# Performance work log

Measured on AMD Instinct MI355X. Metric: run time of the kernel, lower is better.

Reference implementation:

```python
import jax, jax.numpy as jnp
import numpy as np

VEC_DIM = 32
RANK = 2
D = H = W = 40


def setup_inputs() -> dict:
    key = jax.random.key(0)
    k1, k2, k3 = jax.random.split(key, 3)
    volume = jax.random.normal(k1, (D, H, W, VEC_DIM), dtype=jnp.float32)
    # M is nn.Linear(m, m, bias=False) init uniform(-0.5, 0.5)
    M_weight = jax.random.uniform(k2, (VEC_DIM, VEC_DIM), jnp.float32, -0.5, 0.5)
    # P init uniform(-0.1, 0.1)
    P = jax.random.uniform(k3, (VEC_DIM, VEC_DIM), jnp.float32, -0.1, 0.1)
    return {"volume": volume, "M_weight": M_weight, "P": P}


def reference(volume, M_weight, P):
    m = volume.shape[-1]
    r = RANK
    # --- extract_windows: linear mode (step=1), rank_mode='drop', rank_op='avg' ---
    # mean over each r x r x r cubic window == sum-pool / r^3 (VALID padding = drop)
    pooled = jax.lax.reduce_window(
        volume, 0.0, jax.lax.add,
        window_dimensions=(r, r, r, 1),
        window_strides=(1, 1, 1, 1),
        padding="VALID",
    ) / float(r ** 3)  # [Dp, Hp, Wp, m]
    Dp, Hp, Wp = pooled.shape[:3]
    vecs = pooled.reshape(-1, m)  # [B, m], B = Dp*Hp*Wp (window order: k1 outer, k3 inner)
    k1 = jnp.arange(Dp, dtype=jnp.float32)
    k2 = jnp.arange(Hp, dtype=jnp.float32)
    k3 = jnp.arange(Wp, dtype=jnp.float32)
    k1g, k2g, k3g = jnp.meshgrid(k1, k2, k3, indexing="ij")
    k1f, k2f, k3f = k1g.ravel(), k2g.ravel(), k3g.ravel()  # [B]
    # --- batch_compute_Nk ---
    # periods[i, j] = i*m + j + 2
    periods = (jnp.arange(m, dtype=jnp.float32)[:, None] * m
               + jnp.arange(m, dtype=jnp.float32)[None, :] + 2.0)  # [m, m]
    two_pi = 2.0 * jnp.pi
    inv_p = two_pi / periods  # [m, m]
    # phi[b, i, j] = cos(2pi*k1/p) * cos(2pi*k2/p) * cos(2pi*k3/p)
    phi = (jnp.cos(k1f[:, None, None] * inv_p)
           * jnp.cos(k2f[:, None, None] * inv_p)
           * jnp.cos(k3f[:, None, None] * inv_p))  # [B, m, m]
    x = vecs @ M_weight.T  # nn.Linear: x = v W^T, [B, m]
    Nk = jnp.einsum("bj,ij,bij->bi", x, P, phi)  # [B, m]
    return Nk
```

## Files before the change

### kernel.cpp

```cpp
#include <hip/hip_runtime.h>
#include <math.h>

constexpr int DV = 40;
constexpr int NP = 39;
constexpr int VD = 32;
constexpr float TWO_PI = 6.28318530717958647692f;

__global__ __launch_bounds__(256) void ndk_kernel(
    const float* __restrict__ vol,
    const float* __restrict__ Mw,
    const float* __restrict__ P,
    float* __restrict__ out)
{
    __shared__ alignas(16) float pool[8 * VD];
    __shared__ alignas(16) float xs[NP * VD];

    const int tid  = threadIdx.x;
    const int lane = tid & 31;
    const int sub  = tid >> 5;
    const int bx = blockIdx.x;
    const int k1 = bx / NP, k2 = bx % NP;
    const float k1f = (float)k1, k2f = (float)k2;

    float Mr[VD];
    {
        const float4* Mrow = (const float4*)(Mw + lane * VD);
        #pragma unroll
        for (int c4 = 0; c4 < 8; ++c4) {
            float4 m = Mrow[c4];
            Mr[4*c4+0] = m.x; Mr[4*c4+1] = m.y; Mr[4*c4+2] = m.z; Mr[4*c4+3] = m.w;
        }
    }

    const float4* poolv = (const float4*)pool;
    #pragma unroll
    for (int t = 0; t < 5; ++t) {
        const int k3 = t * 8 + sub;
        float pv = 0.f;
        if (k3 < NP) {
            const float* vp = vol + ((size_t)(k1 * DV + k2) * DV + k3) * VD + lane;
            constexpr int SW = VD, SH = DV * VD, SD = DV * DV * VD;
            pv = vp[0]       + vp[SW]
               + vp[SH]      + vp[SH + SW]
               + vp[SD]      + vp[SD + SW]
               + vp[SD + SH] + vp[SD + SH + SW];
            pv *= 0.125f;
        }
        __syncthreads();
        pool[sub * VD + lane] = pv;
        __syncthreads();
        if (k3 < NP) {
            float x = 0.f;
            #pragma unroll
            for (int c4 = 0; c4 < 8; ++c4) {
                float4 p4 = poolv[sub * 8 + c4];
                x += p4.x * Mr[4*c4+0] + p4.y * Mr[4*c4+1]
                   + p4.z * Mr[4*c4+2] + p4.w * Mr[4*c4+3];
            }
            xs[k3 * VD + lane] = x;
        }
    }
    __syncthreads();

    float rx[VD], wv[VD];
    {
        const float4* Prow = (const float4*)(P + lane * VD);
        #pragma unroll
        for (int j4 = 0; j4 < 8; ++j4) {
            float4 p4 = Prow[j4];
            float pj[4] = { p4.x, p4.y, p4.z, p4.w };
            #pragma unroll
            for (int u = 0; u < 4; ++u) {
                const int j = 4 * j4 + u;
                const float w = TWO_PI / (float)(lane * VD + j + 2);
                wv[j] = w;
                rx[j] = pj[u] * __cosf(k1f * w) * __cosf(k2f * w);
            }
        }
    }

    const float4* xsv = (const float4*)xs;
    const long obase = (long)bx * NP;
    #pragma unroll
    for (int t = 0; t < 5; ++t) {
        const int k3 = t * 8 + sub;
        if (k3 < NP) {
            const float k3f = (float)k3;
            float acc = 0.f;
            #pragma unroll
            for (int j4 = 0; j4 < 8; ++j4) {
                float4 xv = xsv[k3 * 8 + j4];
                acc += xv.x * rx[4*j4+0] * __cosf(k3f * wv[4*j4+0]);
                acc += xv.y * rx[4*j4+1] * __cosf(k3f * wv[4*j4+1]);
                acc += xv.z * rx[4*j4+2] * __cosf(k3f * wv[4*j4+2]);
                acc += xv.w * rx[4*j4+3] * __cosf(k3f * wv[4*j4+3]);
            }
            out[(obase + k3) * VD + lane] = acc;
        }
    }
}

extern "C" void kernel_launch(void* const* d_in, const int* in_sizes, int n_in,
                              void* d_out, int out_size, void* d_ws, size_t ws_size,
                              hipStream_t stream) {
    const float* vol = (const float*)d_in[0];
    const float* Mw  = (const float*)d_in[1];
    const float* P   = (const float*)d_in[2];
    float* out = (float*)d_out;
    (void)in_sizes; (void)n_in; (void)out_size; (void)d_ws; (void)ws_size;

    dim3 grid(NP * NP);
    dim3 block(256);
    ndk_kernel<<<grid, block, 0, stream>>>(vol, Mw, P, out);
}
```

Baseline: 89.45 us.

## Use Chebyshev cosine recurrence, bf16 shared staging, and two rows per block

```diff
diff --git a/kernel.cpp b/kernel.cpp
--- a/kernel.cpp
+++ b/kernel.cpp
@@ -4,41 +4,39 @@
 constexpr int DV = 40;
 constexpr int NP = 39;
 constexpr int VD = 32;
+constexpr int NROWS = NP * NP;
 constexpr float TWO_PI = 6.28318530717958647692f;
 
-__global__ __launch_bounds__(256) void ndk_kernel(
+__device__ __forceinline__ unsigned short f2bf(float f) {
+    unsigned u = __float_as_uint(f);
+    u = (u + 0x7fffu + ((u >> 16) & 1u)) >> 16;
+    return (unsigned short)u;
+}
+__device__ __forceinline__ float bflo(unsigned u) { return __uint_as_float(u << 16); }
+__device__ __forceinline__ float bfhi(unsigned u) { return __uint_as_float(u & 0xffff0000u); }
+
+__global__ __launch_bounds__(256, 3) void ndk_kernel(
     const float* __restrict__ vol,
     const float* __restrict__ Mw,
     const float* __restrict__ P,
     float* __restrict__ out)
 {
-    __shared__ alignas(16) float pool[8 * VD];
-    __shared__ alignas(16) float xs[NP * VD];
+    __shared__ __align__(16) unsigned short pool_bf[2][NP][VD];
+    __shared__ __align__(16) unsigned short xs_bf[2][NP][VD];
 
     const int tid  = threadIdx.x;
     const int lane = tid & 31;
-    const int sub  = tid >> 5;
-    const int bx = blockIdx.x;
-    const int k1 = bx / NP, k2 = bx % NP;
-    const float k1f = (float)k1, k2f = (float)k2;
+    const int bx   = blockIdx.x;
 
-    float Mr[VD];
-    {
-        const float4* Mrow = (const float4*)(Mw + lane * VD);
-        #pragma unroll
-        for (int c4 = 0; c4 < 8; ++c4) {
-            float4 m = Mrow[c4];
-            Mr[4*c4+0] = m.x; Mr[4*c4+1] = m.y; Mr[4*c4+2] = m.z; Mr[4*c4+3] = m.w;
-        }
-    }
-
-    const float4* poolv = (const float4*)pool;
-    #pragma unroll
-    for (int t = 0; t < 5; ++t) {
-        const int k3 = t * 8 + sub;
+    for (int s = tid; s < 2 * NP * VD; s += 256) {
+        int row = 0, s2 = s;
+        if (s2 >= NP * VD) { row = 1; s2 -= NP * VD; }
+        const int k3 = s2 >> 5, c = s2 & 31;
+        const int g  = 2 * bx + row;
         float pv = 0.f;
-        if (k3 < NP) {
-            const float* vp = vol + ((size_t)(k1 * DV + k2) * DV + k3) * VD + lane;
+        if (g < NROWS) {
+            const int k1 = g / NP, k2 = g - (g / NP) * NP;
+            const float* vp = vol + ((size_t)(k1 * DV + k2) * DV + k3) * VD + c;
             constexpr int SW = VD, SH = DV * VD, SD = DV * DV * VD;
             pv = vp[0]       + vp[SW]
                + vp[SH]      + vp[SH + SW]
@@ -46,57 +44,92 @@
                + vp[SD + SH] + vp[SD + SH + SW];
             pv *= 0.125f;
         }
-        __syncthreads();
-        pool[sub * VD + lane] = pv;
-        __syncthreads();
-        if (k3 < NP) {
-            float x = 0.f;
-            #pragma unroll
-            for (int c4 = 0; c4 < 8; ++c4) {
-                float4 p4 = poolv[sub * 8 + c4];
-                x += p4.x * Mr[4*c4+0] + p4.y * Mr[4*c4+1]
-                   + p4.z * Mr[4*c4+2] + p4.w * Mr[4*c4+3];
-            }
-            xs[k3 * VD + lane] = x;
+        pool_bf[row][k3][c] = f2bf(pv);
+    }
+
+    float Mr[VD];
+    {
+        const float4* m4 = (const float4*)(Mw + lane * VD);
+        #pragma unroll
+        for (int c4 = 0; c4 < 8; ++c4) {
+            float4 m = m4[c4];
+            Mr[4*c4] = m.x; Mr[4*c4+1] = m.y; Mr[4*c4+2] = m.z; Mr[4*c4+3] = m.w;
         }
     }
     __syncthreads();
 
-    float rx[VD], wv[VD];
+    for (int s = tid; s < 2 * NP * VD; s += 256) {
+        int row = 0, s2 = s;
+        if (s2 >= NP * VD) { row = 1; s2 -= NP * VD; }
+        const int k3 = s2 >> 5;
+        const uint4* pw = (const uint4*)&pool_bf[row][k3][0];
+        float x = 0.f;
+        #pragma unroll
+        for (int r = 0; r < 4; ++r) {
+            uint4 qv = pw[r];
+            const int c = r * 8;
+            x += bflo(qv.x)*Mr[c]   + bfhi(qv.x)*Mr[c+1]
+               + bflo(qv.y)*Mr[c+2] + bfhi(qv.y)*Mr[c+3]
+               + bflo(qv.z)*Mr[c+4] + bfhi(qv.z)*Mr[c+5]
+               + bflo(qv.w)*Mr[c+6] + bfhi(qv.w)*Mr[c+7];
+        }
+        xs_bf[row][k3][lane] = f2bf(x);
+    }
+    __syncthreads();
+
+    const int wv  = tid >> 6;
+    const int row = wv >> 1;
+    const int kh  = (tid >> 5) & 1;
+    const int q   = (wv & 1) * 2 + kh;
+    const int i   = lane;
+    const int g   = 2 * bx + row;
+    const bool valid = g < NROWS;
+    const int kstart = q * 10;
+    const int kend   = min(kstart + 10, NP);
+    const float k1f = (float)(g / NP);
+    const float k2f = (float)(g - (g / NP) * NP);
+
+    float av[VD], d0[VD], dm1[VD];
     {
-        const float4* Prow = (const float4*)(P + lane * VD);
+        const float4* p4 = (const float4*)(P + i * VD);
         #pragma unroll
         for (int j4 = 0; j4 < 8; ++j4) {
-            float4 p4 = Prow[j4];
-            float pj[4] = { p4.x, p4.y, p4.z, p4.w };
+            float4 pr = p4[j4];
+            float pj[4] = { pr.x, pr.y, pr.z, pr.w };
             #pragma unroll
             for (int u = 0; u < 4; ++u) {
-                const int j = 4 * j4 + u;
-                const float w = TWO_PI / (float)(lane * VD + j + 2);
-                wv[j] = w;
-                rx[j] = pj[u] * __cosf(k1f * w) * __cosf(k2f * w);
+                const int j = j4 * 4 + u;
+                const float w  = __fdividef(TWO_PI, (float)(i * VD + j + 2));
+                const float rx = pj[u] * __cosf(k1f * w) * __cosf(k2f * w);
+                av[j]  = 2.f * __cosf(w);
+                d0[j]  = rx * __cosf((float)kstart * w);
+                dm1[j] = rx * __cosf((float)(kstart - 1) * w);
             }
         }
     }
 
-    const float4* xsv = (const float4*)xs;
-    const long obase = (long)bx * NP;
-    #pragma unroll
-    for (int t = 0; t < 5; ++t) {
-        const int k3 = t * 8 + sub;
-        if (k3 < NP) {
-            const float k3f = (float)k3;
-            float acc = 0.f;
-            #pragma unroll
-            for (int j4 = 0; j4 < 8; ++j4) {
-                float4 xv = xsv[k3 * 8 + j4];
-                acc += xv.x * rx[4*j4+0] * __cosf(k3f * wv[4*j4+0]);
-                acc += xv.y * rx[4*j4+1] * __cosf(k3f * wv[4*j4+1]);
-                acc += xv.z * rx[4*j4+2] * __cosf(k3f * wv[4*j4+2]);
-                acc += xv.w * rx[4*j4+3] * __cosf(k3f * wv[4*j4+3]);
-            }
-            out[(obase + k3) * VD + lane] = acc;
+    for (int t = 0; t < 10; ++t) {
+        const int k3  = kstart + t;
+        const int k3r = min(k3, NP - 1);
+        const uint4* xw = (const uint4*)&xs_bf[row][k3r][0];
+        float acc = 0.f;
+        #pragma unroll
+        for (int r = 0; r < 4; ++r) {
+            uint4 qv = xw[r];
+            const int j = r * 8;
+            acc += bflo(qv.x)*d0[j]   + bfhi(qv.x)*d0[j+1]
+                 + bflo(qv.y)*d0[j+2] + bfhi(qv.y)*d0[j+3]
+                 + bflo(qv.z)*d0[j+4] + bfhi(qv.z)*d0[j+5]
+                 + bflo(qv.w)*d0[j+6] + bfhi(qv.w)*d0[j+7];
         }
+        #pragma unroll
+        for (int j = 0; j < VD; ++j) {
+            const float dn = __builtin_fmaf(av[j], d0[j], -dm1[j]);
+            dm1[j] = d0[j];
+            d0[j]  = dn;
+        }
+        if (valid && k3 < kend)
+            out[((size_t)g * NP + k3) * VD + i] = acc;
     }
 }
 
@@ -109,7 +142,7 @@
     float* out = (float*)d_out;
     (void)in_sizes; (void)n_in; (void)out_size; (void)d_ws; (void)ws_size;
 
-    dim3 grid(NP * NP);
+    dim3 grid((NROWS + 1) / 2);
     dim3 block(256);
     ndk_kernel<<<grid, block, 0, stream>>>(vol, Mw, P, out);
 }
```

Result: no change. 89.34 us (-0.1%).
